# Kernel tuning notes

Measured on AMD Instinct MI355X. Metric: run time of the kernel, lower is better.

The kernel has to match this reference:

```python
import jax, jax.numpy as jnp
import numpy as np

B, T, DC, DS, H, V = 8, 1024, 128, 128, 512, 50000
LENGTHS = np.array([2, 4])  # dictionary word lengths for slot 0 and slot 1
LMAX = 4                    # ring-buffer size >= max word length


def setup_inputs() -> dict:
    key = jax.random.key(0)
    ks = jax.random.split(key, 12)
    s = 0.05
    return {
        "char_emb": jax.random.normal(ks[0], (B, T, DC), jnp.float32),
        "word_ids": jax.random.randint(ks[1], (B, T, 2), 0, V),
        "sense_table": jax.random.normal(ks[2], (V, DS), jnp.float32),
        "w_ih": jax.random.normal(ks[3], (DC, 3 * H), jnp.float32) * s,
        "w_hh": jax.random.normal(ks[4], (H, 3 * H), jnp.float32) * s,
        "b": jnp.zeros((3 * H,), jnp.float32),
        "aw_ih": jax.random.normal(ks[5], (DC, H), jnp.float32) * s,
        "aw_hh": jax.random.normal(ks[6], (H, H), jnp.float32) * s,
        "ab": jnp.zeros((H,), jnp.float32),
        "ww_ih": jax.random.normal(ks[7], (DS, 3 * H), jnp.float32) * s,
        "ww_hh": jax.random.normal(ks[8], (H, 3 * H), jnp.float32) * s,
        "wb": jnp.zeros((3 * H,), jnp.float32),
    }


def _forward(char_emb, word_ids, sense_table, w_ih, w_hh, b,
             aw_ih, aw_hh, ab, ww_ih, ww_hh, wb):
    H_ = w_hh.shape[0]
    T_ = char_emb.shape[1]
    lengths = jnp.asarray(LENGTHS)
    slot_idx = jnp.arange(2)

    def run_seq(x_seq, wid_seq):
        # pend: ring buffer of pending word-cell states [LMAX, 2, H]
        def step(carry, t):
            h, c, pend, pmask = carry
            x = x_seq[t]
            # --- MultiInputLSTMCell (char cell) ---
            gates = x @ w_ih + h @ w_hh + b              # [3H]
            i = jax.nn.sigmoid(gates[:H_])
            o = jax.nn.sigmoid(gates[H_:2 * H_])
            g = jnp.tanh(gates[2 * H_:])
            r = jnp.mod(t, LMAX)
            cins = pend[r]                                # [2, H] incoming word cells
            m = pmask[r].astype(x.dtype)                  # [2] validity
            alpha = jax.nn.sigmoid(x @ aw_ih + ab + cins @ aw_hh)  # [2, H]
            ea = jnp.exp(alpha) * m[:, None]
            ei = jnp.exp(i)
            denom = ei + ea.sum(0)
            c_lat = (ei * g + (ea * cins).sum(0)) / denom
            c_plain = (1.0 - i) * c + i * g               # c_num == 0 path: f = 1 - i
            c1 = jnp.where(pmask[r].any(), c_lat, c_plain)
            h1 = o * jnp.tanh(c1)
            # consume the ring slot for this timestep
            pend = pend.at[r].set(0.0)
            pmask = pmask.at[r].set(False)
            # --- WordLSTMCell for words starting at t ---
            xw = sense_table[wid_seq[t]]                  # [2, DS]
            wg = xw @ ww_ih + h1 @ ww_hh + wb             # [2, 3H]
            f = jax.nn.sigmoid(wg[:, :H_])
            iw = jax.nn.sigmoid(wg[:, H_:2 * H_])
            gw = jnp.tanh(wg[:, 2 * H_:])
            cw = f * c1 + iw * gw                         # [2, H]
            ends = t + lengths - 1
            valid = ends < T_
            wslots = jnp.mod(ends, LMAX)
            old = pend[wslots, slot_idx]
            pend = pend.at[wslots, slot_idx].set(jnp.where(valid[:, None], cw, old))
            pmask = pmask.at[wslots, slot_idx].set(valid | pmask[wslots, slot_idx])
            return (h1, c1, pend, pmask), (h1, c1)

        carry0 = (jnp.zeros((H_,), x_seq.dtype), jnp.zeros((H_,), x_seq.dtype),
                  jnp.zeros((LMAX, 2, H_), x_seq.dtype), jnp.zeros((LMAX, 2), bool))
        _, (hs, cs) = jax.lax.scan(step, carry0, jnp.arange(T_))
        return hs, cs

    hs, cs = jax.vmap(run_seq)(char_emb, word_ids)
    return jnp.stack((hs, cs))  # [2, B, T, H]


def reference(char_emb, word_ids, sense_table, w_ih, w_hh, b,
              aw_ih, aw_hh, ab, ww_ih, ww_hh, wb):
    return _forward(char_emb, word_ids, sense_table, w_ih, w_hh, b,
                    aw_ih, aw_hh, ab, ww_ih, ww_hh, wb)
```

## Files before the change

kernel.cpp:

```cpp
#include <hip/hip_runtime.h>
#include <hip/hip_bf16.h>


#define Bq 8
#define Tq 1024
#define DCq 128
#define Hq 512
#define NWG 32
#define NTHR 256

typedef unsigned long long u64;

#define HPUB_OFF  0u
#define PENDP_OFF 65536u
#define WIHT_OFF  327680u
#define WHHT_OFF  720896u
#define AWIHT_OFF 2293760u
#define AWHHT_OFF 2424832u
#define WWIHT_OFF 2949120u
#define WWHHT_OFF 3342336u

__device__ __forceinline__ float bflo(unsigned u){ return __uint_as_float(u << 16); }
__device__ __forceinline__ float bfhi(unsigned u){ return __uint_as_float(u & 0xffff0000u); }
__device__ __forceinline__ float sigm(float x){ return 1.0f / (1.0f + __expf(-x)); }

__device__ __forceinline__ void fma4(float& acc, uint2 w, float4 v){
  acc = fmaf(bflo(w.x), v.x, acc);
  acc = fmaf(bfhi(w.x), v.y, acc);
  acc = fmaf(bflo(w.y), v.z, acc);
  acc = fmaf(bfhi(w.y), v.w, acc);
}

__device__ __forceinline__ float red16(float x){
  x += __shfl_xor(x, 8, 16);
  x += __shfl_xor(x, 4, 16);
  x += __shfl_xor(x, 2, 16);
  x += __shfl_xor(x, 1, 16);
  return x;
}

__device__ __forceinline__ u64 pack64(float v, unsigned gen){
  return ((u64)gen << 32) | (u64)__float_as_uint(v);
}
__device__ __forceinline__ void pub64(u64* p, float v, unsigned gen){
  __hip_atomic_store(p, pack64(v, gen), __ATOMIC_RELAXED, __HIP_MEMORY_SCOPE_AGENT);
}
__device__ __forceinline__ u64 ld64(const u64* p){
  return __hip_atomic_load(p, __ATOMIC_RELAXED, __HIP_MEMORY_SCOPE_AGENT);
}
__device__ __forceinline__ unsigned genof(u64 v){ return (unsigned)(v >> 32); }
__device__ __forceinline__ float valof(u64 v){ return __uint_as_float((unsigned)v); }

__global__ void transpose_bf16(const float* __restrict__ src, __hip_bfloat16* __restrict__ dst,
                               int kshift, int total, int N){
  const int K = 1 << kshift;
  for (int idx = blockIdx.x * blockDim.x + threadIdx.x; idx < total;
       idx += gridDim.x * blockDim.x){
    int n = idx >> kshift;
    int k = idx & (K - 1);
    dst[idx] = __float2bfloat16(src[(size_t)k * N + n]);
  }
}

__global__ void __launch_bounds__(NTHR, 1)
lattice_main(const float* __restrict__ char_emb,
             const int*   __restrict__ word_ids,
             const float* __restrict__ sense_table,
             const float* __restrict__ bias_b,
             const float* __restrict__ bias_ab,
             const float* __restrict__ bias_wb,
             unsigned char* __restrict__ ws,
             float* __restrict__ out)
{
  const int seq  = blockIdx.x;
  const int wg   = blockIdx.y;
  const int tid  = threadIdx.x;
  const int grp  = tid >> 4;
  const int lane = tid & 15;
  const int J    = wg * 16 + grp;
  const int i0   = tid * 2, i1 = tid * 2 + 1;

  u64* hpub = (u64*)(ws + HPUB_OFF)  + (size_t)seq * 2 * Hq;
  u64* pnd  = (u64*)(ws + PENDP_OFF) + (size_t)seq * 4 * 2 * Hq;

  const uint2* w_ihT  = (const uint2*)(ws + WIHT_OFF);
  const uint2* w_hhT  = (const uint2*)(ws + WHHT_OFF);
  const uint2* aw_ihT = (const uint2*)(ws + AWIHT_OFF);
  const uint2* aw_hhT = (const uint2*)(ws + AWHHT_OFF);
  const uint2* ww_ihT = (const uint2*)(ws + WWIHT_OFF);
  const uint2* ww_hhT = (const uint2*)(ws + WWHHT_OFF);

  uint2 Rwhh_i[8], Rwhh_o[8], Rwhh_g[8], Rawhh[8];
  uint2 Rwwh_f[8], Rwwh_i[8], Rwwh_g[8];
  uint2 Rwih_i[2], Rwih_o[2], Rwih_g[2], Rawih[2];
  uint2 Rwwi_f[2], Rwwi_i[2], Rwwi_g[2];
  {
    const uint2* whh_i = w_hhT  + (size_t)(0*Hq + J) * 128;
    const uint2* whh_o = w_hhT  + (size_t)(1*Hq + J) * 128;
    const uint2* whh_g = w_hhT  + (size_t)(2*Hq + J) * 128;
    const uint2* awhh  = aw_hhT + (size_t)J * 128;
    const uint2* wwh_f = ww_hhT + (size_t)(0*Hq + J) * 128;
    const uint2* wwh_i = ww_hhT + (size_t)(1*Hq + J) * 128;
    const uint2* wwh_g = ww_hhT + (size_t)(2*Hq + J) * 128;
#pragma unroll
    for (int it = 0; it < 8; ++it){
      const int q = it * 16 + lane;
      Rwhh_i[it] = whh_i[q];  Rwhh_o[it] = whh_o[q];  Rwhh_g[it] = whh_g[q];
      Rawhh[it]  = awhh[q];
      Rwwh_f[it] = wwh_f[q];  Rwwh_i[it] = wwh_i[q];  Rwwh_g[it] = wwh_g[q];
    }
    const uint2* wih_i = w_ihT  + (size_t)(0*Hq + J) * 32;
    const uint2* wih_o = w_ihT  + (size_t)(1*Hq + J) * 32;
    const uint2* wih_g = w_ihT  + (size_t)(2*Hq + J) * 32;
    const uint2* awih  = aw_ihT + (size_t)J * 32;
    const uint2* wwi_f = ww_ihT + (size_t)(0*Hq + J) * 32;
    const uint2* wwi_i = ww_ihT + (size_t)(1*Hq + J) * 32;
    const uint2* wwi_g = ww_ihT + (size_t)(2*Hq + J) * 32;
#pragma unroll
    for (int it = 0; it < 2; ++it){
      const int q = it * 16 + lane;
      Rwih_i[it] = wih_i[q];  Rwih_o[it] = wih_o[q];  Rwih_g[it] = wih_g[q];
      Rawih[it]  = awih[q];
      Rwwi_f[it] = wwi_f[q];  Rwwi_i[it] = wwi_i[q];  Rwwi_g[it] = wwi_g[q];
    }
  }

  const float b_i  = bias_b[J], b_o = bias_b[Hq + J], b_g = bias_b[2*Hq + J];
  const float ab_J = bias_ab[J];
  const float wb_f = bias_wb[J], wb_i = bias_wb[Hq + J], wb_g = bias_wb[2*Hq + J];

  float* out_h = out + (size_t)seq * Tq * Hq;
  float* out_c = out + ((size_t)Bq + seq) * Tq * Hq;

  __shared__ __align__(16) float shH[2][Hq];
  __shared__ __align__(16) float sh_p0[Hq];
  __shared__ __align__(16) float sh_p1[Hq];
  __shared__ __align__(16) float shx[2][DCq];
  __shared__ __align__(16) float shxw0[2][DCq];
  __shared__ __align__(16) float shxw1[2][DCq];

  shH[0][i0] = 0.f; shH[0][i1] = 0.f;
  shH[1][i0] = 0.f; shH[1][i1] = 0.f;
  sh_p0[i0] = 0.f; sh_p0[i1] = 0.f;
  sh_p1[i0] = 0.f; sh_p1[i1] = 0.f;
  if (tid < DCq){
    shx[0][tid] = char_emb[((size_t)seq * Tq + 0) * DCq + tid];
  } else {
    const int k = tid - DCq;
    const int w0 = word_ids[(size_t)seq * Tq * 2 + 0];
    const int w1 = word_ids[(size_t)seq * Tq * 2 + 1];
    shxw0[0][k] = sense_table[(size_t)w0 * DCq + k];
    shxw1[0][k] = sense_table[(size_t)w1 * DCq + k];
  }
  __syncthreads();

  for (int t = 0; t < Tq; ++t){
    const int par = t & 1;
    const float* hprev = shH[par ^ 1];

    float a_i = 0.f, a_o = 0.f, a_g = 0.f, a_xa = 0.f;
#pragma unroll
    for (int it = 0; it < 8; ++it){
      const int k0 = it * 64 + lane * 4;
      float4 hv = *(const float4*)(hprev + k0);
      fma4(a_i, Rwhh_i[it], hv);
      fma4(a_o, Rwhh_o[it], hv);
      fma4(a_g, Rwhh_g[it], hv);
    }
#pragma unroll
    for (int it = 0; it < 2; ++it){
      const int k0 = it * 64 + lane * 4;
      float4 xv = *(const float4*)(shx[par] + k0);
      fma4(a_i,  Rwih_i[it], xv);
      fma4(a_o,  Rwih_o[it], xv);
      fma4(a_g,  Rwih_g[it], xv);
      fma4(a_xa, Rawih[it],  xv);
    }

    if (t >= 3){
      const u64* p0 = pnd + ((size_t)(t & 3) * 2 + 0) * Hq;
      const u64* p1 = pnd + ((size_t)(t & 3) * 2 + 1) * Hq;
      const unsigned tg0 = (unsigned)t, tg1 = (unsigned)(t - 2);
      u64 a, b, c, d;
      for (;;){
        a = ld64(p0 + i0); b = ld64(p0 + i1);
        c = ld64(p1 + i0); d = ld64(p1 + i1);
        if (genof(a) >= tg0 && genof(b) >= tg0 &&
            genof(c) >= tg1 && genof(d) >= tg1) break;
      }
      sh_p0[i0] = valof(a); sh_p0[i1] = valof(b);
      sh_p1[i0] = valof(c); sh_p1[i1] = valof(d);
    } else if (t >= 1){
      const u64* p0 = pnd + ((size_t)(t & 3) * 2 + 0) * Hq;
      const unsigned tg0 = (unsigned)t;
      u64 a, b;
      for (;;){
        a = ld64(p0 + i0); b = ld64(p0 + i1);
        if (genof(a) >= tg0 && genof(b) >= tg0) break;
      }
      sh_p0[i0] = valof(a); sh_p0[i1] = valof(b);
    }
    __syncthreads();

    float a_p0 = 0.f, a_p1 = 0.f;
#pragma unroll
    for (int it = 0; it < 8; ++it){
      const int k0 = it * 64 + lane * 4;
      float4 p0v = *(const float4*)(sh_p0 + k0);
      float4 p1v = *(const float4*)(sh_p1 + k0);
      fma4(a_p0, Rawhh[it], p0v);
      fma4(a_p1, Rawhh[it], p1v);
    }
    a_i  = red16(a_i);  a_o  = red16(a_o);  a_g  = red16(a_g);
    a_xa = red16(a_xa); a_p0 = red16(a_p0); a_p1 = red16(a_p1);

    const float gi = sigm(a_i + b_i);
    const float go = sigm(a_o + b_o);
    const float gg = tanhf(a_g + b_g);
    float c1;
    if (t == 0){
      c1 = gi * gg;
    } else {
      const float base = a_xa + ab_J;
      const float ea0 = __expf(sigm(base + a_p0));
      const float ei  = __expf(gi);
      float num = ei * gg + ea0 * sh_p0[J];
      float den = ei + ea0;
      if (t >= 3){
        const float ea1 = __expf(sigm(base + a_p1));
        num += ea1 * sh_p1[J];
        den += ea1;
      }
      c1 = num / den;
    }
    const float h1 = go * tanhf(c1);
    if (lane == 0){
      pub64(hpub + (size_t)par * Hq + J, h1, (unsigned)(t + 1));
      out_h[(size_t)t * Hq + J] = h1;
      out_c[(size_t)t * Hq + J] = c1;
    }

    {
      const int tn = (t + 1 < Tq) ? t + 1 : t;
      if (tid < DCq){
        shx[par ^ 1][tid] = char_emb[((size_t)seq * Tq + tn) * DCq + tid];
      } else {
        const int k = tid - DCq;
        const int w0 = word_ids[((size_t)seq * Tq + tn) * 2 + 0];
        const int w1 = word_ids[((size_t)seq * Tq + tn) * 2 + 1];
        shxw0[par ^ 1][k] = sense_table[(size_t)w0 * DCq + k];
        shxw1[par ^ 1][k] = sense_table[(size_t)w1 * DCq + k];
      }
      const u64* hp = hpub + (size_t)par * Hq;
      const unsigned tg = (unsigned)(t + 1);
      u64 a, b;
      for (;;){
        a = ld64(hp + i0); b = ld64(hp + i1);
        if (genof(a) >= tg && genof(b) >= tg) break;
      }
      shH[par][i0] = valof(a); shH[par][i1] = valof(b);
    }
    __syncthreads();

    float r_f = 0.f, r_i = 0.f, r_g = 0.f;
    float x_f0 = 0.f, x_i0 = 0.f, x_g0 = 0.f, x_f1 = 0.f, x_i1 = 0.f, x_g1 = 0.f;
#pragma unroll
    for (int it = 0; it < 8; ++it){
      const int k0 = it * 64 + lane * 4;
      float4 hv = *(const float4*)(shH[par] + k0);
      fma4(r_f, Rwwh_f[it], hv);
      fma4(r_i, Rwwh_i[it], hv);
      fma4(r_g, Rwwh_g[it], hv);
    }
#pragma unroll
    for (int it = 0; it < 2; ++it){
      const int k0 = it * 64 + lane * 4;
      float4 x0 = *(const float4*)(shxw0[par] + k0);
      float4 x1 = *(const float4*)(shxw1[par] + k0);
      fma4(x_f0, Rwwi_f[it], x0);  fma4(x_f1, Rwwi_f[it], x1);
      fma4(x_i0, Rwwi_i[it], x0);  fma4(x_i1, Rwwi_i[it], x1);
      fma4(x_g0, Rwwi_g[it], x0);  fma4(x_g1, Rwwi_g[it], x1);
    }
    r_f  = red16(r_f);  r_i  = red16(r_i);  r_g  = red16(r_g);
    x_f0 = red16(x_f0); x_i0 = red16(x_i0); x_g0 = red16(x_g0);
    x_f1 = red16(x_f1); x_i1 = red16(x_i1); x_g1 = red16(x_g1);

    if (lane == 0){
      const float f0  = sigm(r_f + x_f0 + wb_f);
      const float iw0 = sigm(r_i + x_i0 + wb_i);
      const float g0  = tanhf(r_g + x_g0 + wb_g);
      const float cw0 = f0 * c1 + iw0 * g0;
      const float f1  = sigm(r_f + x_f1 + wb_f);
      const float iw1 = sigm(r_i + x_i1 + wb_i);
      const float g1  = tanhf(r_g + x_g1 + wb_g);
      const float cw1 = f1 * c1 + iw1 * g1;
      pub64(pnd + ((size_t)((t + 1) & 3) * 2 + 0) * Hq + J, cw0, (unsigned)(t + 1));
      pub64(pnd + ((size_t)((t + 3) & 3) * 2 + 1) * Hq + J, cw1, (unsigned)(t + 1));
    }
  }
}

extern "C" void kernel_launch(void* const* d_in, const int* in_sizes, int n_in,
                              void* d_out, int out_size, void* d_ws, size_t ws_size,
                              hipStream_t stream){
  const float* char_emb = (const float*)d_in[0];
  const int*   word_ids = (const int*)d_in[1];
  const float* sense    = (const float*)d_in[2];
  const float* w_ih     = (const float*)d_in[3];
  const float* w_hh     = (const float*)d_in[4];
  const float* bb       = (const float*)d_in[5];
  const float* aw_ih    = (const float*)d_in[6];
  const float* aw_hh    = (const float*)d_in[7];
  const float* ab       = (const float*)d_in[8];
  const float* ww_ih    = (const float*)d_in[9];
  const float* ww_hh    = (const float*)d_in[10];
  const float* wb       = (const float*)d_in[11];
  unsigned char* ws = (unsigned char*)d_ws;
  float* out = (float*)d_out;

  hipMemsetAsync(ws, 0, WIHT_OFF, stream);

  transpose_bf16<<<512, NTHR, 0, stream>>>(w_ih,  (__hip_bfloat16*)(ws + WIHT_OFF),  7, 128*1536, 1536);
  transpose_bf16<<<512, NTHR, 0, stream>>>(w_hh,  (__hip_bfloat16*)(ws + WHHT_OFF),  9, 512*1536, 1536);
  transpose_bf16<<<512, NTHR, 0, stream>>>(aw_ih, (__hip_bfloat16*)(ws + AWIHT_OFF), 7, 128*512,  512);
  transpose_bf16<<<512, NTHR, 0, stream>>>(aw_hh, (__hip_bfloat16*)(ws + AWHHT_OFF), 9, 512*512,  512);
  transpose_bf16<<<512, NTHR, 0, stream>>>(ww_ih, (__hip_bfloat16*)(ws + WWIHT_OFF), 7, 128*1536, 1536);
  transpose_bf16<<<512, NTHR, 0, stream>>>(ww_hh, (__hip_bfloat16*)(ws + WWHHT_OFF), 9, 512*1536, 1536);

  dim3 grid(Bq, NWG);
  lattice_main<<<grid, NTHR, 0, stream>>>(char_emb, word_ids, sense, bb, ab, wb, ws, out);
}
```

Before: 5.607 ms.

## Prefetch pending flags early and hoist independent matvecs before spin-waits

Issues the loads of the pending word-cell flags at the top of each step so they overlap the h@W_hh matvec. The x-dependent reductions and the word-input matvec now run before the cross-workgroup waits, taking them off the critical path. Spin loops use volatile loads and fall back to an agent-scope atomic load every eighth iteration. Publishing now writes each value twice, once through a volatile store and once atomically. Volatile loads may hit stale cache lines and spin longer, and the extra store adds memory traffic.

```diff
diff --git a/kernel.cpp b/kernel.cpp
--- a/kernel.cpp
+++ b/kernel.cpp
@@ -43,10 +43,15 @@
   return ((u64)gen << 32) | (u64)__float_as_uint(v);
 }
 __device__ __forceinline__ void pub64(u64* p, float v, unsigned gen){
-  __hip_atomic_store(p, pack64(v, gen), __ATOMIC_RELAXED, __HIP_MEMORY_SCOPE_AGENT);
+  u64 w = pack64(v, gen);
+  *(volatile u64*)p = w;
+  __hip_atomic_store(p, w, __ATOMIC_RELAXED, __HIP_MEMORY_SCOPE_AGENT);
 }
 __device__ __forceinline__ u64 ld64(const u64* p){
   return __hip_atomic_load(p, __ATOMIC_RELAXED, __HIP_MEMORY_SCOPE_AGENT);
+}
+__device__ __forceinline__ u64 vld64(const u64* p){
+  return *(volatile const u64*)p;
 }
 __device__ __forceinline__ unsigned genof(u64 v){ return (unsigned)(v >> 32); }
 __device__ __forceinline__ float valof(u64 v){ return __uint_as_float((unsigned)v); }
@@ -158,6 +163,12 @@
     const int par = t & 1;
     const float* hprev = shH[par ^ 1];
 
+    const u64* p0 = pnd + ((size_t)(t & 3) * 2 + 0) * Hq;
+    const u64* p1 = pnd + ((size_t)(t & 3) * 2 + 1) * Hq;
+    u64 qa = 0, qb = 0, qc = 0, qd = 0;
+    if (t >= 1){ qa = vld64(p0 + i0); qb = vld64(p0 + i1); }
+    if (t >= 3){ qc = vld64(p1 + i0); qd = vld64(p1 + i1); }
+
     float a_i = 0.f, a_o = 0.f, a_g = 0.f, a_xa = 0.f;
 #pragma unroll
     for (int it = 0; it < 8; ++it){
@@ -176,29 +187,34 @@
       fma4(a_g,  Rwih_g[it], xv);
       fma4(a_xa, Rawih[it],  xv);
     }
+    a_i  = red16(a_i);  a_o  = red16(a_o);  a_g  = red16(a_g);  a_xa = red16(a_xa);
 
     if (t >= 3){
-      const u64* p0 = pnd + ((size_t)(t & 3) * 2 + 0) * Hq;
-      const u64* p1 = pnd + ((size_t)(t & 3) * 2 + 1) * Hq;
       const unsigned tg0 = (unsigned)t, tg1 = (unsigned)(t - 2);
-      u64 a, b, c, d;
-      for (;;){
-        a = ld64(p0 + i0); b = ld64(p0 + i1);
-        c = ld64(p1 + i0); d = ld64(p1 + i1);
-        if (genof(a) >= tg0 && genof(b) >= tg0 &&
-            genof(c) >= tg1 && genof(d) >= tg1) break;
-      }
-      sh_p0[i0] = valof(a); sh_p0[i1] = valof(b);
-      sh_p1[i0] = valof(c); sh_p1[i1] = valof(d);
+      int itc = 0;
+      while (!(genof(qa) >= tg0 && genof(qb) >= tg0 &&
+               genof(qc) >= tg1 && genof(qd) >= tg1)){
+        if ((++itc & 7) == 0){
+          qa = ld64(p0 + i0);  qb = ld64(p0 + i1);
+          qc = ld64(p1 + i0);  qd = ld64(p1 + i1);
+        } else {
+          qa = vld64(p0 + i0); qb = vld64(p0 + i1);
+          qc = vld64(p1 + i0); qd = vld64(p1 + i1);
+        }
+      }
+      sh_p0[i0] = valof(qa); sh_p0[i1] = valof(qb);
+      sh_p1[i0] = valof(qc); sh_p1[i1] = valof(qd);
     } else if (t >= 1){
-      const u64* p0 = pnd + ((size_t)(t & 3) * 2 + 0) * Hq;
       const unsigned tg0 = (unsigned)t;
-      u64 a, b;
-      for (;;){
-        a = ld64(p0 + i0); b = ld64(p0 + i1);
-        if (genof(a) >= tg0 && genof(b) >= tg0) break;
-      }
-      sh_p0[i0] = valof(a); sh_p0[i1] = valof(b);
+      int itc = 0;
+      while (!(genof(qa) >= tg0 && genof(qb) >= tg0)){
+        if ((++itc & 7) == 0){
+          qa = ld64(p0 + i0);  qb = ld64(p0 + i1);
+        } else {
+          qa = vld64(p0 + i0); qb = vld64(p0 + i1);
+        }
+      }
+      sh_p0[i0] = valof(qa); sh_p0[i1] = valof(qb);
     }
     __syncthreads();
 
@@ -211,8 +227,7 @@
       fma4(a_p0, Rawhh[it], p0v);
       fma4(a_p1, Rawhh[it], p1v);
     }
-    a_i  = red16(a_i);  a_o  = red16(a_o);  a_g  = red16(a_g);
-    a_xa = red16(a_xa); a_p0 = red16(a_p0); a_p1 = red16(a_p1);
+    a_p0 = red16(a_p0); a_p1 = red16(a_p1);
 
     const float gi = sigm(a_i + b_i);
     const float go = sigm(a_o + b_o);
@@ -240,6 +255,18 @@
       out_c[(size_t)t * Hq + J] = c1;
     }
 
+    float x_f0 = 0.f, x_i0 = 0.f, x_g0 = 0.f, x_f1 = 0.f, x_i1 = 0.f, x_g1 = 0.f;
+#pragma unroll
+    for (int it = 0; it < 2; ++it){
+      const int k0 = it * 64 + lane * 4;
+      float4 x0 = *(const float4*)(shxw0[par] + k0);
+      float4 x1 = *(const float4*)(shxw1[par] + k0);
+      fma4(x_f0, Rwwi_f[it], x0);  fma4(x_f1, Rwwi_f[it], x1);
+      fma4(x_i0, Rwwi_i[it], x0);  fma4(x_i1, Rwwi_i[it], x1);
+      fma4(x_g0, Rwwi_g[it], x0);  fma4(x_g1, Rwwi_g[it], x1);
+    }
+    x_f0 = red16(x_f0); x_i0 = red16(x_i0); x_g0 = red16(x_g0);
+    x_f1 = red16(x_f1); x_i1 = red16(x_i1); x_g1 = red16(x_g1);
     {
       const int tn = (t + 1 < Tq) ? t + 1 : t;
       if (tid < DCq){
@@ -251,19 +278,25 @@
         shxw0[par ^ 1][k] = sense_table[(size_t)w0 * DCq + k];
         shxw1[par ^ 1][k] = sense_table[(size_t)w1 * DCq + k];
       }
+    }
+
+    {
       const u64* hp = hpub + (size_t)par * Hq;
       const unsigned tg = (unsigned)(t + 1);
-      u64 a, b;
-      for (;;){
-        a = ld64(hp + i0); b = ld64(hp + i1);
-        if (genof(a) >= tg && genof(b) >= tg) break;
+      u64 a = vld64(hp + i0), b = vld64(hp + i1);
+      int itc = 0;
+      while (!(genof(a) >= tg && genof(b) >= tg)){
+        if ((++itc & 7) == 0){
+          a = ld64(hp + i0);  b = ld64(hp + i1);
+        } else {
+          a = vld64(hp + i0); b = vld64(hp + i1);
+        }
       }
       shH[par][i0] = valof(a); shH[par][i1] = valof(b);
     }
     __syncthreads();
 
     float r_f = 0.f, r_i = 0.f, r_g = 0.f;
-    float x_f0 = 0.f, x_i0 = 0.f, x_g0 = 0.f, x_f1 = 0.f, x_i1 = 0.f, x_g1 = 0.f;
 #pragma unroll
     for (int it = 0; it < 8; ++it){
       const int k0 = it * 64 + lane * 4;
@@ -272,18 +305,7 @@
       fma4(r_i, Rwwh_i[it], hv);
       fma4(r_g, Rwwh_g[it], hv);
     }
-#pragma unroll
-    for (int it = 0; it < 2; ++it){
-      const int k0 = it * 64 + lane * 4;
-      float4 x0 = *(const float4*)(shxw0[par] + k0);
-      float4 x1 = *(const float4*)(shxw1[par] + k0);
-      fma4(x_f0, Rwwi_f[it], x0);  fma4(x_f1, Rwwi_f[it], x1);
-      fma4(x_i0, Rwwi_i[it], x0);  fma4(x_i1, Rwwi_i[it], x1);
-      fma4(x_g0, Rwwi_g[it], x0);  fma4(x_g1, Rwwi_g[it], x1);
-    }
-    r_f  = red16(r_f);  r_i  = red16(r_i);  r_g  = red16(r_g);
-    x_f0 = red16(x_f0); x_i0 = red16(x_i0); x_g0 = red16(x_g0);
-    x_f1 = red16(x_f1); x_i1 = red16(x_i1); x_g1 = red16(x_g1);
+    r_f = red16(r_f); r_i = red16(r_i); r_g = red16(r_g);
 
     if (lane == 0){
       const float f0  = sigm(r_f + x_f0 + wb_f);
```

Result: slower. 7.817 ms (+39.4%).
